# Performance work log

Measured on AMD Instinct MI355X. Metric: run time of the kernel, lower is better.

## Reference

```python
import jax, jax.numpy as jnp
import numpy as np

EPS = 1e-6

def _ln(x):
    m = jnp.mean(x, axis=-1, keepdims=True)
    v = jnp.mean((x - m) ** 2, axis=-1, keepdims=True)
    return (x - m) * jax.lax.rsqrt(v + EPS)

def _quant(x):
    # dynamic per-token symmetric int8 quant (fused_kernels.quant_sum semantics)
    s = jnp.maximum(jnp.max(jnp.abs(x), axis=-1, keepdims=True) / 127.0, 1e-8)
    q = jnp.clip(jnp.round(x / s), -127.0, 127.0)
    return q, s, jnp.sum(q, axis=-1, keepdims=True)

def _w8a8(x, qw, sw, zw, b):
    # W8A8OF16LinearDynamicInputScale: int8 GEMM + zero-point correction via row sum
    q, s, qsum = _quant(x)
    acc = q @ qw.astype(jnp.float32).T - qsum * zw.astype(jnp.float32)
    return acc * (s * sw) + b

def _self_attn(xm, Wqkv, bqkv, Wo, bo, H):
    Bt, S, C = xm.shape
    hd = C // H
    qkv = (xm @ Wqkv.T + bqkv).reshape(Bt, S, 3, H, hd)
    q, k, v = qkv[:, :, 0], qkv[:, :, 1], qkv[:, :, 2]
    attn = jnp.einsum('bqhd,bkhd->bhqk', q * (hd ** -0.5), k).astype(jnp.float32)
    attn = jax.nn.softmax(attn, axis=-1)
    out = jnp.einsum('bhqk,bkhd->bqhd', attn, v).reshape(Bt, S, C)
    return out @ Wo.T + bo

def _cross_attn(x, y, qw_q, sw_q, zw_q, b_q, Wkv, bkv, qw_cp, sw_cp, zw_cp, b_cp, H):
    B, N, C = x.shape
    hd = C // H
    q = _w8a8(x, qw_q, sw_q, zw_q, b_q).reshape(B * N, H, hd)
    kv = (y.reshape(-1, C) @ Wkv.T + bkv).reshape(-1, 2, H, hd)
    k, v = kv[:, 0], kv[:, 1]
    # mask=None path: q (1,B*N,H,hd) attends over all B*M keys (flattened)
    attn = jnp.einsum('qhd,khd->hqk', q * (hd ** -0.5), k).astype(jnp.float32)
    attn = jax.nn.softmax(attn, axis=-1)
    out = jnp.einsum('hqk,khd->qhd', attn, v).reshape(B, N, C)
    return _w8a8(out, qw_cp, sw_cp, zw_cp, b_cp)

def setup_inputs() -> dict:
    key = jax.random.key(0)
    ks = iter(jax.random.split(key, 32))
    B, T, S, C, H, M = 2, 8, 256, 1152, 16, 224
    Dh = int(C * 4.0)
    r = lambda shape, sc=1.0: jax.random.normal(next(ks), shape, dtype=jnp.float32) * sc
    qi = lambda shape: jax.random.randint(next(ks), shape, -127, 128, dtype=jnp.int8)
    zi = lambda shape: jax.random.randint(next(ks), shape, -8, 9, dtype=jnp.int32)
    su = lambda shape: jax.random.uniform(next(ks), shape, minval=0.005, maxval=0.02, dtype=jnp.float32)
    return dict(
        x=r((B, T * S, C)), y=r((B, M, C)), t=r((B, 6 * C)),
        sst=r((6, C), C ** -0.5),
        Wqkv=r((3 * C, C), 0.02), bqkv=r((3 * C,), 0.02),
        Wo=r((C, C), 0.02), bo=r((C,), 0.02),
        Wkv=r((2 * C, C), 0.02), bkv=r((2 * C,), 0.02),
        qw_q=qi((C, C)), sw_q=su((C,)), zw_q=zi((C,)), b_q=r((C,), 0.02),
        qw_cp=qi((C, C)), sw_cp=su((C,)), zw_cp=zi((C,)), b_cp=r((C,), 0.02),
        qw_f1=qi((Dh, C)), sw_f1=su((Dh,)), zw_f1=zi((Dh,)), b_f1=r((Dh,), 0.02),
        qw_f2=qi((C, Dh)), sw_f2=su((C,)), zw_f2=zi((C,)), b_f2=r((C,), 0.02),
        num_heads=H, T=T, S=S,
    )

def reference(x, y, t, sst, Wqkv, bqkv, Wo, bo, Wkv, bkv,
              qw_q, sw_q, zw_q, b_q, qw_cp, sw_cp, zw_cp, b_cp,
              qw_f1, sw_f1, zw_f1, b_f1, qw_f2, sw_f2, zw_f2, b_f2,
              num_heads, T, S):
    B, N, C = x.shape
    mod = sst[None] + t.reshape(B, 6, C)  # (B,6,C)
    shift_msa, scale_msa, gate_msa, shift_mlp, scale_mlp, gate_mlp = (
        mod[:, 0:1], mod[:, 1:2], mod[:, 2:3], mod[:, 3:4], mod[:, 4:5], mod[:, 5:6])
    # --- self-attention (spatial, temporal=False): B (T S) C -> (B T) S C ---
    x_m = _ln(x) * (1.0 + scale_msa) + shift_msa
    x_m = x_m.reshape(B * T, S, C)
    x_m = _self_attn(x_m, Wqkv, bqkv, Wo, bo, num_heads).reshape(B, N, C)
    x = x + gate_msa * x_m  # fused_kernels.gate_residual
    # --- int8 cross-attention ---
    x = x + _cross_attn(x, y, qw_q, sw_q, zw_q, b_q, Wkv, bkv, qw_cp, sw_cp, zw_cp, b_cp, num_heads)
    # --- int8 MLP with fused gelu_quant_sum (tanh-approx GELU) ---
    x_m = _ln(x) * (1.0 + scale_mlp) + shift_mlp
    h = _w8a8(x_m, qw_f1, sw_f1, zw_f1, b_f1)
    h = jax.nn.gelu(h, approximate=True)
    h = _w8a8(h, qw_f2, sw_f2, zw_f2, b_f2)
    x = x + gate_mlp * h
    return x
```

## Files before the change

kernel.cpp:

```cpp
#include <hip/hip_runtime.h>
#include <stdint.h>

typedef unsigned short u16;
typedef _Float16 f16;
typedef f16    f16v8  __attribute__((ext_vector_type(8)));
typedef u16    u16v8  __attribute__((ext_vector_type(8)));
typedef float  f32x4  __attribute__((ext_vector_type(4)));
typedef int    i32x4  __attribute__((ext_vector_type(4)));
typedef int    i32x16 __attribute__((ext_vector_type(16)));

#define MFMA_F16(a,b,c)   __builtin_amdgcn_mfma_f32_16x16x32_f16((a),(b),(c),0,0,0)
#define MFMA_I8_32(a,b,c) __builtin_amdgcn_mfma_i32_32x32x32_i8((a),(b),(c),0,0,0)

__device__ __forceinline__ float b2f(u16 u){ union{unsigned u;float f;}v; v.u=((unsigned)u)<<16; return v.f; }
__device__ __forceinline__ u16 f2b(float f){ union{float f;unsigned u;}v; v.f=f;
  return (u16)((v.u + 0x7fffu + ((v.u>>16)&1u))>>16); }
__device__ __forceinline__ u16 f2h(float f){ f16 h = (f16)f; return __builtin_bit_cast(u16, h); }
__device__ __forceinline__ float h2f(u16 u){ return (float)__builtin_bit_cast(f16, u); }
__device__ __forceinline__ f16v8 ldh8(const u16* p){ return __builtin_bit_cast(f16v8, *(const u16v8*)p); }
__device__ __forceinline__ void gl2lds16(const void* g, void* l){
  __builtin_amdgcn_global_load_lds(
    (const __attribute__((address_space(1))) unsigned int*)g,
    (__attribute__((address_space(3))) unsigned int*)l,
    16, 0, 0);
}
__device__ __forceinline__ float gelu_t(float x){
  float t = tanhf(0.7978845608028654f*(x + 0.044715f*x*x*x));
  return 0.5f*x*(1.0f+t);
}

__global__ void mod_add_k(const float* __restrict__ sst, const float* __restrict__ t, float* __restrict__ mod){
  int i = blockIdx.x*256 + threadIdx.x;
  if (i < 2*6*1152) mod[i] = sst[i % 6912] + t[i];
}
__global__ void split2h_k(const float* __restrict__ src, u16* __restrict__ hi, u16* __restrict__ lo, int n){
  int i = blockIdx.x*256 + threadIdx.x;
  if (i >= n) return;
  float v = src[i];
  f16 h = (f16)v;
  hi[i] = __builtin_bit_cast(u16, h);
  lo[i] = f2h(v - (float)h);
}
__global__ void cross_prep_k(const int* __restrict__ qw_q, int8_t* __restrict__ w8q,
                             const int* __restrict__ qw_cp, int8_t* __restrict__ w8cp,
                             const float* __restrict__ Wkv, u16* __restrict__ wkvh, u16* __restrict__ wkvl,
                             const float* __restrict__ y, u16* __restrict__ yf){
  const int S1 = 1327104, S2 = 2654208, S3 = 5308416, S4 = 5824512;
  int i = blockIdx.x*256 + threadIdx.x;
  if (i < S1){ w8q[i] = (int8_t)qw_q[i]; }
  else if (i < S2){ int j = i - S1; w8cp[j] = (int8_t)qw_cp[j]; }
  else if (i < S3){ int j = i - S2; float v = Wkv[j]; f16 h = (f16)v;
    wkvh[j] = __builtin_bit_cast(u16, h); wkvl[j] = f2h(v - (float)h); }
  else if (i < S4){ int j = i - S3; yf[j] = f2h(y[j]); }
}
__global__ void mlp_prep_k(const int* __restrict__ qw_f1, int8_t* __restrict__ w8f1,
                           const int* __restrict__ qw_f2, int8_t* __restrict__ w8f2){
  const int S1 = 5308416, S2 = 10616832;
  int i = blockIdx.x*256 + threadIdx.x;
  if (i < S1){ w8f1[i] = (int8_t)qw_f1[i]; }
  else if (i < S2){ int j = i - S1; w8f2[j] = (int8_t)qw_f2[j]; }
}
__global__ void ln_mod_f16_k(const float* __restrict__ src, u16* __restrict__ xf,
                             const float* __restrict__ mod, int shift_row, int scale_row){
  const int row = blockIdx.x, tid = threadIdx.x;
  const int b = row >> 11;
  const float* ms = mod + ((size_t)b*6 + shift_row)*1152;
  const float* mc = mod + ((size_t)b*6 + scale_row)*1152;
  __shared__ float r1[256], r2[256];
  float s = 0.f, sq = 0.f, vals[5]; int cnt = 0;
  for (int c = tid; c < 1152; c += 256){
    float v = src[(size_t)row*1152+c];
    vals[cnt++] = v; s += v; sq += v*v;
  }
  r1[tid]=s; r2[tid]=sq; __syncthreads();
  for (int st=128; st>0; st>>=1){ if (tid<st){ r1[tid]+=r1[tid+st]; r2[tid]+=r2[tid+st]; } __syncthreads(); }
  float mean = r1[0]*(1.f/1152.f);
  float var  = r2[0]*(1.f/1152.f) - mean*mean;
  float rstd = rsqrtf(var + 1e-6f);
  cnt = 0;
  for (int c = tid; c < 1152; c += 256){
    float v = (vals[cnt++]-mean)*rstd*(1.f+mc[c]) + ms[c];
    xf[(size_t)row*1152+c] = f2h(v);
  }
}
__global__ void rgq_k(const float* __restrict__ x, const float* __restrict__ ao,
                      const float* __restrict__ mod, int gate_row, float* __restrict__ xw,
                      int8_t* __restrict__ q8, float* __restrict__ s_out, int* __restrict__ q_out){
  const int row = blockIdx.x, tid = threadIdx.x;
  const int b = row >> 11;
  const float* mg = mod + ((size_t)b*6 + gate_row)*1152;
  __shared__ float r1[256];
  __shared__ int ri[256];
  float mx = 0.f, vals[5]; int cnt = 0;
  for (int c = tid; c < 1152; c += 256){
    float v = x[(size_t)row*1152+c] + mg[c]*ao[(size_t)row*1152+c];
    xw[(size_t)row*1152+c] = v;
    vals[cnt++] = v; mx = fmaxf(mx, fabsf(v));
  }
  r1[tid]=mx; __syncthreads();
  for (int st=128; st>0; st>>=1){ if (tid<st) r1[tid]=fmaxf(r1[tid],r1[tid+st]); __syncthreads(); }
  const float s_ = fmaxf(r1[0]*(1.f/127.f), 1e-8f);
  const float inv = 1.f/s_;
  int acc = 0; cnt = 0;
  for (int c = tid; c < 1152; c += 256){
    float q = rintf(vals[cnt++]*inv);
    q = fminf(fmaxf(q, -127.f), 127.f);
    q8[(size_t)row*1152+c] = (int8_t)q;
    acc += (int)q;
  }
  ri[tid]=acc; __syncthreads();
  for (int st=128; st>0; st>>=1){ if (tid<st) ri[tid]+=ri[tid+st]; __syncthreads(); }
  if (tid==0){ s_out[row]=s_; q_out[row]=ri[0]; }
}
__global__ void rlq_k(float* __restrict__ xw, const float* __restrict__ add,
                      const float* __restrict__ mod, int shift_row, int scale_row,
                      int8_t* __restrict__ q8, float* __restrict__ s_out, int* __restrict__ q_out){
  const int row = blockIdx.x, tid = threadIdx.x;
  const int b = row >> 11;
  const float* ms = mod + ((size_t)b*6 + shift_row)*1152;
  const float* mc = mod + ((size_t)b*6 + scale_row)*1152;
  __shared__ float r1[256], r2[256];
  __shared__ int ri[256];
  float s = 0.f, sq = 0.f, vals[5]; int cnt = 0;
  for (int c = tid; c < 1152; c += 256){
    float v = xw[(size_t)row*1152+c] + add[(size_t)row*1152+c];
    xw[(size_t)row*1152+c] = v;
    vals[cnt++] = v; s += v; sq += v*v;
  }
  r1[tid]=s; r2[tid]=sq; __syncthreads();
  for (int st=128; st>0; st>>=1){ if (tid<st){ r1[tid]+=r1[tid+st]; r2[tid]+=r2[tid+st]; } __syncthreads(); }
  float mean = r1[0]*(1.f/1152.f);
  float var  = r2[0]*(1.f/1152.f) - mean*mean;
  float rstd = rsqrtf(var + 1e-6f);
  __syncthreads();
  float mx = 0.f; cnt = 0;
  for (int c = tid; c < 1152; c += 256){
    float v = (vals[cnt]-mean)*rstd*(1.f+mc[c]) + ms[c];
    vals[cnt++] = v; mx = fmaxf(mx, fabsf(v));
  }
  r1[tid]=mx; __syncthreads();
  for (int st=128; st>0; st>>=1){ if (tid<st) r1[tid]=fmaxf(r1[tid],r1[tid+st]); __syncthreads(); }
  const float s_ = fmaxf(r1[0]*(1.f/127.f), 1e-8f);
  const float inv = 1.f/s_;
  int acc = 0; cnt = 0;
  for (int c = tid; c < 1152; c += 256){
    float q = rintf(vals[cnt++]*inv);
    q = fminf(fmaxf(q, -127.f), 127.f);
    q8[(size_t)row*1152+c] = (int8_t)q;
    acc += (int)q;
  }
  ri[tid]=acc; __syncthreads();
  for (int st=128; st>0; st>>=1){ if (tid<st) ri[tid]+=ri[tid+st]; __syncthreads(); }
  if (tid==0){ s_out[row]=s_; q_out[row]=ri[0]; }
}
template<int SRC_F32>
__global__ void quant_rows_k(const void* __restrict__ src, int C_,
                             int8_t* __restrict__ q8, float* __restrict__ s_out, int* __restrict__ q_out){
  const int row = blockIdx.x, tid = threadIdx.x;
  __shared__ float red[256];
  __shared__ int redi[256];
  float vals[18];
  float mx = 0.f; int cnt = 0;
  for (int c = tid; c < C_; c += 256){
    float v = SRC_F32 ? ((const float*)src)[(size_t)row*C_+c] : b2f(((const u16*)src)[(size_t)row*C_+c]);
    vals[cnt++] = v;
    mx = fmaxf(mx, fabsf(v));
  }
  red[tid]=mx; __syncthreads();
  for (int st=128; st>0; st>>=1){ if (tid<st) red[tid]=fmaxf(red[tid],red[tid+st]); __syncthreads(); }
  const float s_ = fmaxf(red[0]*(1.f/127.f), 1e-8f);
  const float inv = 1.f/s_;
  int acc = 0; cnt = 0;
  for (int c = tid; c < C_; c += 256){
    float q = rintf(vals[cnt++]*inv);
    q = fminf(fmaxf(q, -127.f), 127.f);
    q8[(size_t)row*C_+c] = (int8_t)q;
    acc += (int)q;
  }
  redi[tid]=acc; __syncthreads();
  for (int st=128; st>0; st>>=1){ if (tid<st) redi[tid]+=redi[tid+st]; __syncthreads(); }
  if (tid==0){ s_out[row]=s_; q_out[row]=redi[0]; }
}

template<int MODE>
__global__ __launch_bounds__(256,4) void gemm_f16k(
    const u16* __restrict__ Af, int lda,
    const u16* __restrict__ Wh, const u16* __restrict__ Wl, int ldw,
    const float* __restrict__ bias, float* __restrict__ out, int ldo, int M, int K,
    u16* __restrict__ e1, u16* __restrict__ e2){
  __shared__ u16 sA[128*32];
  __shared__ u16 sWh[128*32];
  __shared__ u16 sWl[128*32];
  const int tid = threadIdx.x, lane = tid & 63;
  const int wv = tid >> 6, wx = wv & 1, wy = wv >> 1;
  const int quad = lane >> 4, l16 = lane & 15;
  const int m0 = blockIdx.y*128, n0 = blockIdx.x*128;
  f32x4 acc[4][4];
  #pragma unroll
  for (int i=0;i<4;i++)
    #pragma unroll
    for (int j=0;j<4;j++) acc[i][j] = (f32x4){0.f,0.f,0.f,0.f};
  for (int k0=0; k0<K; k0+=32){
    #pragma unroll
    for (int r=0;r<2;r++){
      int slotbase = r*256 + wv*64;
      int slot = slotbase + lane;
      int row = slot >> 2;
      int col8 = ((slot ^ (row>>1)) & 3) * 8;
      int gm = m0 + row; if (gm > M-1) gm = M-1;
      size_t aoff = (size_t)gm*lda + k0 + col8;
      size_t woff = (size_t)(n0+row)*ldw + k0 + col8;
      gl2lds16(Af + aoff, &sA[(size_t)slotbase*8]);
      gl2lds16(Wh + woff, &sWh[(size_t)slotbase*8]);
      gl2lds16(Wl + woff, &sWl[(size_t)slotbase*8]);
    }
    __syncthreads();
    const int cs = ((quad ^ ((l16>>1)&3)) * 8);
    f16v8 a[4], bh[4], bl[4];
    #pragma unroll
    for (int i=0;i<4;i++) a[i] = ldh8(&sA[(wy*64+i*16+l16)*32 + cs]);
    #pragma unroll
    for (int j=0;j<4;j++){
      bh[j] = ldh8(&sWh[(wx*64+j*16+l16)*32 + cs]);
      bl[j] = ldh8(&sWl[(wx*64+j*16+l16)*32 + cs]);
    }
    #pragma unroll
    for (int i=0;i<4;i++)
      #pragma unroll
      for (int j=0;j<4;j++){
        acc[i][j] = MFMA_F16(a[i], bh[j], acc[i][j]);
        acc[i][j] = MFMA_F16(a[i], bl[j], acc[i][j]);
      }
    __syncthreads();
  }
  #pragma unroll
  for (int j=0;j<4;j++){
    int col = n0 + wx*64 + j*16 + l16;
    float bc = bias ? bias[col] : 0.f;
    #pragma unroll
    for (int i=0;i<4;i++)
      #pragma unroll
      for (int r=0;r<4;r++){
        int row = m0 + wy*64 + i*16 + quad*4 + r;
        if (row >= M) continue;
        float v = acc[i][j][r] + bc;
        if (MODE == 0){
          out[(size_t)row*ldo + col] = v;
        } else if (MODE == 1){
          if (col < 2304){
            e1[(size_t)row*2304 + col] = f2h(v);
          } else {
            int vc = col - 2304;
            int hd_ = vc/72, d = vc - hd_*72;
            int z = row >> 8, s2 = row & 255;
            e2[((size_t)(z*16+hd_)*80 + d)*256 + s2] = f2h(v);
          }
        } else {
          if (col < 1152){
            e1[(size_t)row*1152 + col] = f2h(v);
          } else {
            int vc = col - 1152;
            int hd_ = vc/72, d = vc - hd_*72;
            e2[((size_t)hd_*80 + d)*448 + row] = f2h(v);
          }
        }
      }
  }
}

#define QKV_NT 36
__global__ __launch_bounds__(512,2) void gemm_qkv_8ph(
    const u16* __restrict__ Af,
    const u16* __restrict__ Wh_, const u16* __restrict__ Wl_,
    const float* __restrict__ bias,
    u16* __restrict__ qkf, u16* __restrict__ vtf){
  extern __shared__ u16 sm[];
  char* smb = (char*)sm;
  const int tid = threadIdx.x, lane = tid & 63, wv = tid >> 6;
  const int wr = wv >> 2, wc = wv & 3;
  const int quad = lane >> 4, l16 = lane & 15;
  const int c = blockIdx.x & 7, bi = blockIdx.x >> 3;
  const int m0 = (((c>>1)<<2) + (bi&3)) << 8;
  const int n0 = ((c&1)*7 + (bi>>2)) << 8;

  const u16* gA[2]; const u16* gH[2]; const u16* gL[2];
  int sbase[2];
  #pragma unroll
  for (int r=0;r<2;r++){
    int slot = r*512 + tid;
    int row = slot >> 2;
    int col8 = ((slot ^ (row>>1)) & 3) * 8;
    sbase[r] = (r*512 + wv*64) * 16;
    gA[r] = Af + (size_t)(m0+row)*1152 + col8;
    int gn = n0 + row; if (gn > 3455) gn = 3455;
    gH[r] = Wh_ + (size_t)gn*1152 + col8;
    gL[r] = Wl_ + (size_t)gn*1152 + col8;
  }

  #define STG_A(t2,b) { size_t ko=(size_t)(t2)*32; \
    gl2lds16(gA[0]+ko, smb + (b)*49152 + sbase[0]); \
    gl2lds16(gA[1]+ko, smb + (b)*49152 + sbase[1]); }
  #define STG_H(t2,b) { size_t ko=(size_t)(t2)*32; \
    gl2lds16(gH[0]+ko, smb + (b)*49152 + 16384 + sbase[0]); \
    gl2lds16(gH[1]+ko, smb + (b)*49152 + 16384 + sbase[1]); }
  #define STG_L(t2,b) { size_t ko=(size_t)(t2)*32; \
    gl2lds16(gL[0]+ko, smb + (b)*49152 + 32768 + sbase[0]); \
    gl2lds16(gL[1]+ko, smb + (b)*49152 + 32768 + sbase[1]); }

  STG_A(0,0); STG_H(0,0); STG_L(0,0);
  STG_A(1,1); STG_H(1,1); STG_L(1,1);

  const int cs = (quad ^ ((l16>>1)&3)) * 8;
  const int arow = wr*128 + l16;
  const int wrow = wc*64 + l16;

  f32x4 acc[8][4];
  #pragma unroll
  for (int i=0;i<8;i++)
    #pragma unroll
    for (int j=0;j<4;j++) acc[i][j] = (f32x4){0.f,0.f,0.f,0.f};

  f16v8 bh[4], bl[4];

  #define PHASE(p, STAGE_STMT) { \
    const u16* bA = sm + cur*24576; \
    f16v8 a0 = ldh8(bA + (arow + (2*(p))*16)*32 + cs); \
    f16v8 a1 = ldh8(bA + (arow + (2*(p)+1)*16)*32 + cs); \
    if ((p)==0){ \
      const u16* bH = bA + 8192; \
      const u16* bL = bA + 16384; \
      _Pragma("unroll") \
      for (int j=0;j<4;j++){ \
        bh[j] = ldh8(bH + (wrow + j*16)*32 + cs); \
        bl[j] = ldh8(bL + (wrow + j*16)*32 + cs); \
      } \
    } \
    STAGE_STMT; \
    __builtin_amdgcn_s_barrier(); \
    asm volatile("s_waitcnt lgkmcnt(0)" ::: "memory"); \
    __builtin_amdgcn_sched_barrier(0); \
    __builtin_amdgcn_s_setprio(1); \
    _Pragma("unroll") \
    for (int j=0;j<4;j++){ \
      acc[2*(p)][j]   = MFMA_F16(a0, bh[j], acc[2*(p)][j]); \
      acc[2*(p)][j]   = MFMA_F16(a0, bl[j], acc[2*(p)][j]); \
      acc[2*(p)+1][j] = MFMA_F16(a1, bh[j], acc[2*(p)+1][j]); \
      acc[2*(p)+1][j] = MFMA_F16(a1, bl[j], acc[2*(p)+1][j]); \
    } \
    __builtin_amdgcn_s_setprio(0); \
    __builtin_amdgcn_s_barrier(); \
  }

  int cur = 0;
  for (int t = 0; t < QKV_NT-1; ++t){
    const int nxt = (cur == 0) ? 2 : cur - 1;
    asm volatile("s_waitcnt vmcnt(6)" ::: "memory");
    __builtin_amdgcn_s_barrier();
    __builtin_amdgcn_sched_barrier(0);
    const bool pf = (t < QKV_NT-2);
    PHASE(0, if (pf) STG_A(t+2,nxt));
    PHASE(1, if (pf) STG_H(t+2,nxt));
    PHASE(2, if (pf) STG_L(t+2,nxt));
    PHASE(3, );
    cur = (cur == 2) ? 0 : cur + 1;
  }
  asm volatile("s_waitcnt vmcnt(0)" ::: "memory");
  __builtin_amdgcn_s_barrier();
  __builtin_amdgcn_sched_barrier(0);
  PHASE(0, );
  PHASE(1, );
  PHASE(2, );
  PHASE(3, );

  #pragma unroll
  for (int j=0;j<4;j++){
    const int col = n0 + wc*64 + j*16 + l16;
    if (col < 3456){
      const float bc = bias[col];
      if (col < 2304){
        #pragma unroll
        for (int i=0;i<8;i++){
          const size_t rb = (size_t)(m0 + wr*128 + i*16 + quad*4)*2304 + col;
          #pragma unroll
          for (int r=0;r<4;r++)
            qkf[rb + (size_t)r*2304] = f2h(acc[i][j][r] + bc);
        }
      } else {
        const int vc = col - 2304;
        const int hd_ = vc/72, d = vc - hd_*72;
        #pragma unroll
        for (int i=0;i<8;i++){
          #pragma unroll
          for (int r=0;r<4;r++){
            const int row = m0 + wr*128 + i*16 + quad*4 + r;
            const int z = row >> 8, s2 = row & 255;
            vtf[((size_t)(z*16+hd_)*80 + d)*256 + s2] = f2h(acc[i][j][r] + bc);
          }
        }
      }
    }
  }
  #undef PHASE
  #undef STG_A
  #undef STG_H
  #undef STG_L
}

__global__ __launch_bounds__(256,3) void gemm_i8(
    const int8_t* __restrict__ A, int lda, const int8_t* __restrict__ W, int ldw,
    const float* __restrict__ rs, const int* __restrict__ rq,
    const float* __restrict__ sw, const int* __restrict__ zw, const float* __restrict__ bias,
    void* __restrict__ out, int ldo, int M, int K, int do_gelu, int out_f32,
    const float* __restrict__ xwf, const float* __restrict__ modf, int do_final){
  __shared__ int8_t As[128*128];
  __shared__ int8_t Bs[128*128];
  const int tid = threadIdx.x, lane = tid & 63, wv = tid >> 6;
  const int wx = wv & 1, wy = wv >> 1;
  const int l32 = lane & 31, g = lane >> 5;
  const int m0 = blockIdx.y*128, n0 = blockIdx.x*128;
  const int srow = lane >> 3, schunk = lane & 7;
  const int scol = ((schunk ^ srow) & 7) * 16;
  i32x16 acc[2][2];
  #pragma unroll
  for (int i=0;i<2;i++)
    #pragma unroll
    for (int j=0;j<2;j++)
      #pragma unroll
      for (int r=0;r<16;r++) acc[i][j][r] = 0;
  for (int k0 = 0; k0 < K; k0 += 128){
    #pragma unroll
    for (int i=0;i<4;i++){
      int rr = (i*4 + wv)*8;
      int gm = m0 + rr + srow; if (gm > M-1) gm = M-1;
      gl2lds16(A + (size_t)gm*lda + k0 + scol, &As[rr*128]);
      int gn = n0 + rr + srow;
      gl2lds16(W + (size_t)gn*ldw + k0 + scol, &Bs[rr*128]);
    }
    __syncthreads();
    #pragma unroll
    for (int kq=0; kq<4; kq++){
      i32x4 af[2], bw[2];
      #pragma unroll
      for (int i=0;i<2;i++){
        int row = wy*64 + i*32 + l32;
        int cs = (((kq*2 + g) ^ (row & 7))) * 16;
        af[i] = *(const i32x4*)&As[row*128 + cs];
      }
      #pragma unroll
      for (int j=0;j<2;j++){
        int row = wx*64 + j*32 + l32;
        int cs = (((kq*2 + g) ^ (row & 7))) * 16;
        bw[j] = *(const i32x4*)&Bs[row*128 + cs];
      }
      #pragma unroll
      for (int i=0;i<2;i++)
        #pragma unroll
        for (int j=0;j<2;j++)
          acc[i][j] = MFMA_I8_32(af[i], bw[j], acc[i][j]);
    }
    __syncthreads();
  }
  #pragma unroll
  for (int j=0;j<2;j++){
    int col = n0 + wx*64 + j*32 + l32;
    float swc = sw[col]; float zwc = (float)zw[col]; float bc = bias[col];
    #pragma unroll
    for (int i=0;i<2;i++)
      #pragma unroll
      for (int r=0;r<16;r++){
        int row = m0 + wy*64 + i*32 + (r&3) + 8*(r>>2) + 4*g;
        if (row < M){
          float v = ((float)acc[i][j][r] - (float)rq[row]*zwc) * (rs[row]*swc) + bc;
          if (do_gelu) v = gelu_t(v);
          if (do_final){
            int bb = row >> 11;
            float ov = xwf[(size_t)row*1152 + col] + modf[((size_t)bb*6+5)*1152 + col]*v;
            ((float*)out)[(size_t)row*ldo + col] = ov;
          } else if (out_f32) ((float*)out)[(size_t)row*ldo + col] = v;
          else                ((u16*)out)[(size_t)row*ldo + col] = f2b(v);
        }
      }
  }
}

__global__ __launch_bounds__(256) void attn_self_f16(
    const u16* __restrict__ qkf, const u16* __restrict__ vtf,
    u16* __restrict__ of, float scale){
  constexpr int NT = 16, PSTR = 264, VSTR = 256;
  __shared__ u16 P[4*16*PSTR];
  const int tid = threadIdx.x, lane = tid & 63, wv = tid >> 6;
  const int quad = lane >> 4, l16 = lane & 15;
  const int h = blockIdx.y, z = blockIdx.z;
  const int qbase = z*256 + blockIdx.x*64;
  const u16* Vth = vtf + (size_t)(z*16+h)*80*VSTR;
  const f16v8 zf = __builtin_bit_cast(f16v8, (u16v8)0);
  const int mrow = qbase + wv*16 + l16;

  f16v8 qf[3];
  #pragma unroll
  for (int t=0;t<3;t++){
    if (t==2 && quad!=0){ qf[t]=zf; }
    else qf[t] = ldh8(qkf + (size_t)mrow*2304 + h*72 + t*32 + (t==2?0:quad*8));
  }
  f32x4 sc[NT];
  #pragma unroll
  for (int nt=0; nt<NT; nt++){
    f32x4 a = {0.f,0.f,0.f,0.f};
    #pragma unroll
    for (int t=0;t<3;t++){
      f16v8 kf = zf;
      if (!(t==2 && quad!=0))
        kf = ldh8(qkf + (size_t)(z*256 + nt*16 + l16)*2304 + 1152 + h*72 + t*32 + (t==2?0:quad*8));
      a = MFMA_F16(qf[t], kf, a);
    }
    sc[nt] = a;
  }
  float mx[4] = {-1e30f,-1e30f,-1e30f,-1e30f};
  #pragma unroll
  for (int nt=0; nt<NT; nt++)
    #pragma unroll
    for (int r=0;r<4;r++){ float v = sc[nt][r]*scale; sc[nt][r]=v; mx[r]=fmaxf(mx[r],v); }
  #pragma unroll
  for (int r=0;r<4;r++)
    for (int d=1; d<16; d<<=1) mx[r] = fmaxf(mx[r], __shfl_xor(mx[r], d, 64));
  float sm[4] = {0.f,0.f,0.f,0.f};
  #pragma unroll
  for (int nt=0; nt<NT; nt++)
    #pragma unroll
    for (int r=0;r<4;r++){ float p = __expf(sc[nt][r]-mx[r]); sc[nt][r]=p; sm[r]+=p; }
  #pragma unroll
  for (int r=0;r<4;r++){
    for (int d=1; d<16; d<<=1) sm[r] += __shfl_xor(sm[r], d, 64);
    sm[r] = 1.f/sm[r];
  }
  u16* Pw = P + wv*16*PSTR;
  #pragma unroll
  for (int nt=0; nt<NT; nt++)
    #pragma unroll
    for (int r=0;r<4;r++)
      Pw[(quad*4+r)*PSTR + nt*16 + l16] = f2h(sc[nt][r]*sm[r]);
  const u16* Pr = P + wv*16*PSTR + (size_t)l16*PSTR;
  #pragma unroll
  for (int dt=0; dt<5; dt++){
    f32x4 o = {0.f,0.f,0.f,0.f};
    #pragma unroll
    for (int kk=0; kk<8; kk++){
      f16v8 pv = ldh8(Pr + kk*32 + quad*8);
      f16v8 bv = ldh8(Vth + (size_t)(dt*16+l16)*VSTR + kk*32 + quad*8);
      o = MFMA_F16(pv, bv, o);
    }
    int d = dt*16 + l16;
    if (d < 72){
      #pragma unroll
      for (int r=0;r<4;r++){
        int row = qbase + wv*16 + quad*4 + r;
        of[(size_t)row*1152 + h*72 + d] = f2h(o[r]);
      }
    }
  }
}

__global__ __launch_bounds__(256) void attn_cross_f16(
    const float* __restrict__ Q32,
    const u16* __restrict__ Kf,
    const u16* __restrict__ Vt,
    float* __restrict__ O, float scale){
  constexpr int NT = 28, PSTR = 456, VSTR = 448;
  __shared__ u16 P[4*16*PSTR];
  const int tid = threadIdx.x, lane = tid & 63, wv = tid >> 6;
  const int quad = lane >> 4, l16 = lane & 15;
  const int h = blockIdx.y;
  const int qbase = blockIdx.x*64;
  const u16* Vth = Vt + (size_t)h*80*VSTR;
  const f16v8 zf = __builtin_bit_cast(f16v8, (u16v8)0);

  const int mrow = qbase + wv*16 + l16;
  const float* qp = Q32 + (size_t)mrow*1152 + h*72;
  f16v8 qf[3];
  #pragma unroll
  for (int t=0;t<3;t++){
    if (t==2 && quad!=0){ qf[t]=zf; continue; }
    u16v8 hv;
    #pragma unroll
    for (int j=0;j<8;j++) hv[j] = f2h(qp[t*32 + (t==2?0:quad*8) + j]);
    qf[t] = __builtin_bit_cast(f16v8, hv);
  }
  f32x4 sc[NT];
  #pragma unroll
  for (int nt=0; nt<NT; nt++){
    f32x4 a = {0.f,0.f,0.f,0.f};
    #pragma unroll
    for (int t=0;t<3;t++){
      f16v8 kf = zf;
      if (!(t==2 && quad!=0))
        kf = ldh8(Kf + (size_t)(nt*16 + l16)*1152 + h*72 + t*32 + (t==2?0:quad*8));
      a = MFMA_F16(qf[t], kf, a);
    }
    sc[nt] = a;
  }
  float mx[4] = {-1e30f,-1e30f,-1e30f,-1e30f};
  #pragma unroll
  for (int nt=0; nt<NT; nt++)
    #pragma unroll
    for (int r=0;r<4;r++){ float v = sc[nt][r]*scale; sc[nt][r]=v; mx[r]=fmaxf(mx[r],v); }
  #pragma unroll
  for (int r=0;r<4;r++)
    for (int d=1; d<16; d<<=1) mx[r] = fmaxf(mx[r], __shfl_xor(mx[r], d, 64));
  float sm[4] = {0.f,0.f,0.f,0.f};
  #pragma unroll
  for (int nt=0; nt<NT; nt++)
    #pragma unroll
    for (int r=0;r<4;r++){ float p = __expf(sc[nt][r]-mx[r]); sc[nt][r]=p; sm[r]+=p; }
  #pragma unroll
  for (int r=0;r<4;r++){
    for (int d=1; d<16; d<<=1) sm[r] += __shfl_xor(sm[r], d, 64);
    sm[r] = 1.f/sm[r];
  }
  u16* Pw = P + wv*16*PSTR;
  #pragma unroll
  for (int nt=0; nt<NT; nt++)
    #pragma unroll
    for (int r=0;r<4;r++)
      Pw[(quad*4+r)*PSTR + nt*16 + l16] = f2h(sc[nt][r]*sm[r]);
  const u16* Pr = P + wv*16*PSTR + (size_t)l16*PSTR;
  #pragma unroll
  for (int dt=0; dt<5; dt++){
    f32x4 o = {0.f,0.f,0.f,0.f};
    #pragma unroll
    for (int kk=0; kk<14; kk++){
      f16v8 pv = ldh8(Pr + kk*32 + quad*8);
      f16v8 bv = ldh8(Vth + (size_t)(dt*16+l16)*VSTR + kk*32 + quad*8);
      o = MFMA_F16(pv, bv, o);
    }
    int d = dt*16 + l16;
    if (d < 72){
      #pragma unroll
      for (int r=0;r<4;r++){
        int row = qbase + wv*16 + quad*4 + r;
        O[(size_t)row*1152 + h*72 + d] = o[r];
      }
    }
  }
}

extern "C" void kernel_launch(void* const* d_in, const int* in_sizes, int n_in,
                              void* d_out, int out_size, void* d_ws, size_t ws_size,
                              hipStream_t stream){
  const float* x    = (const float*)d_in[0];
  const float* y    = (const float*)d_in[1];
  const float* t    = (const float*)d_in[2];
  const float* sst  = (const float*)d_in[3];
  const float* Wqkv = (const float*)d_in[4];
  const float* bqkv = (const float*)d_in[5];
  const float* Wo   = (const float*)d_in[6];
  const float* bo   = (const float*)d_in[7];
  const float* Wkv  = (const float*)d_in[8];
  const float* bkv  = (const float*)d_in[9];
  const int*   qw_q  = (const int*)d_in[10];
  const float* sw_q  = (const float*)d_in[11];
  const int*   zw_q  = (const int*)d_in[12];
  const float* b_q   = (const float*)d_in[13];
  const int*   qw_cp = (const int*)d_in[14];
  const float* sw_cp = (const float*)d_in[15];
  const int*   zw_cp = (const int*)d_in[16];
  const float* b_cp  = (const float*)d_in[17];
  const int*   qw_f1 = (const int*)d_in[18];
  const float* sw_f1 = (const float*)d_in[19];
  const int*   zw_f1 = (const int*)d_in[20];
  const float* b_f1  = (const float*)d_in[21];
  const int*   qw_f2 = (const int*)d_in[22];
  const float* sw_f2 = (const float*)d_in[23];
  const int*   zw_f2 = (const int*)d_in[24];
  const float* b_f2  = (const float*)d_in[25];
  (void)in_sizes; (void)n_in; (void)out_size;

  constexpr size_t SZR = (size_t)4096*1152*4;
  constexpr size_t R0 = 0;
  constexpr size_t R1 = R0 + SZR;
  constexpr size_t R2 = R1 + SZR;
  constexpr size_t R3 = R2 + SZR;
  constexpr size_t R4 = R3 + SZR;
  constexpr size_t R5 = R4 + (size_t)9437184;
  constexpr size_t R6 = R5 + (size_t)9437184;
  constexpr size_t RS = R6 + (size_t)10485760;
  constexpr size_t RQ = RS + (size_t)4096*4;
  constexpr size_t RM = RQ + (size_t)4096*4;
  constexpr size_t WS_NEED = RM + (size_t)2*6*1152*4;
  if (ws_size < WS_NEED) return;

  char* ws = (char*)d_ws;
  float*  xw    = (float*)(ws + R0);
  u16*    wqkvh = (u16*)(ws + R1);
  u16*    wqkvl = (u16*)(ws + R1 + (size_t)3456*1152*2);
  u16*    wkvh  = (u16*)(ws + R1);
  u16*    wkvl  = (u16*)(ws + R1 + (size_t)2304*1152*2);
  u16*    yf    = (u16*)(ws + R1 + (size_t)2*2304*1152*2);
  float*  q32   = (float*)(ws + R1);
  float*  cpout = (float*)(ws + R1);
  int8_t* q8h   = (int8_t*)(ws + R1);
  u16*    qkf   = (u16*)(ws + R2);
  float*  aof   = (float*)(ws + R2);
  u16*    hbuf  = (u16*)(ws + R2);
  u16*    xmf   = (u16*)(ws + R4);
  u16*    of    = (u16*)(ws + R4);
  u16*    kf    = (u16*)(ws + R4 + (size_t)4128768);
  u16*    vtc   = (u16*)(ws + R4 + (size_t)6193152);
  int8_t* w8f2  = (int8_t*)(ws + R4);
  int8_t* w8q   = (int8_t*)(ws + R5);
  int8_t* w8cp  = (int8_t*)(ws + R5 + (size_t)1327104);
  int8_t* w8f1  = (int8_t*)(ws + R5 + (size_t)2654208);
  u16*    vtf   = (u16*)(ws + R6);
  u16*    woh   = (u16*)(ws + R6);
  u16*    wol   = (u16*)(ws + R6 + (size_t)1152*1152*2);
  int8_t* q8x   = (int8_t*)(ws + R6);
  float*  rs    = (float*)(ws + RS);
  int*    rq    = (int*)(ws + RQ);
  float*  mod   = (float*)(ws + RM);

  const float scale = 0.11785113019775793f;

  static bool attr_set = false;
  if (!attr_set){
    hipFuncSetAttribute(reinterpret_cast<const void*>(gemm_qkv_8ph),
                        hipFuncAttributeMaxDynamicSharedMemorySize, 3*49152);
    attr_set = true;
  }

  mod_add_k<<<(2*6*1152+255)/256,256,0,stream>>>(sst, t, mod);

  ln_mod_f16_k<<<4096,256,0,stream>>>(x, xmf, mod, 0, 1);
  split2h_k<<<(3456*1152+255)/256,256,0,stream>>>(Wqkv, wqkvh, wqkvl, 3456*1152);
  gemm_qkv_8ph<<<dim3(224),dim3(512),3*49152,stream>>>(xmf, wqkvh, wqkvl, bqkv, qkf, vtf);
  attn_self_f16<<<dim3(4,16,16),256,0,stream>>>(qkf, vtf, of, scale);
  split2h_k<<<(1152*1152+255)/256,256,0,stream>>>(Wo, woh, wol, 1152*1152);
  gemm_f16k<0><<<dim3(9,32),256,0,stream>>>(of,1152, woh,wol,1152, bo, aof,1152, 4096,1152, nullptr,nullptr);
  rgq_k<<<4096,256,0,stream>>>(x, aof, mod, 2, xw, q8x, rs, rq);

  cross_prep_k<<<(5824512+255)/256,256,0,stream>>>(qw_q,w8q, qw_cp,w8cp, Wkv,wkvh,wkvl, y,yf);
  gemm_f16k<2><<<dim3(18,4),256,0,stream>>>(yf,1152, wkvh,wkvl,1152, bkv, nullptr,0, 448,1152, kf,vtc);
  gemm_i8<<<dim3(9,32),256,0,stream>>>(q8x,1152, w8q,1152, rs,rq, sw_q,zw_q,b_q, q32,1152, 4096,1152, 0, 1, nullptr,nullptr,0);
  attn_cross_f16<<<dim3(64,16),256,0,stream>>>(q32, kf, vtc, aof, scale);
  quant_rows_k<1><<<4096,256,0,stream>>>(aof, 1152, q8x, rs, rq);
  gemm_i8<<<dim3(9,32),256,0,stream>>>(q8x,1152, w8cp,1152, rs,rq, sw_cp,zw_cp,b_cp, cpout,1152, 4096,1152, 0, 1, nullptr,nullptr,0);

  rlq_k<<<4096,256,0,stream>>>(xw, cpout, mod, 3, 4, q8x, rs, rq);
  mlp_prep_k<<<(10616832+255)/256,256,0,stream>>>(qw_f1, w8f1, qw_f2, w8f2);
  gemm_i8<<<dim3(36,32),256,0,stream>>>(q8x,1152, w8f1,1152, rs,rq, sw_f1,zw_f1,b_f1, hbuf,4608, 4096,1152, 1, 0, nullptr,nullptr,0);
  quant_rows_k<0><<<4096,256,0,stream>>>(hbuf, 4608, q8h, rs, rq);
  gemm_i8<<<dim3(9,32),256,0,stream>>>(q8h,4608, w8f2,4608, rs,rq, sw_f2,zw_f2,b_f2, d_out,1152, 4096,4608, 0, 1, xw,mod,1);
}
```

Before: 791.5 us.

## Double-buffer int8 GEMM LDS tiles with async prefetch of next K-slab

The int8 GEMM now keeps two LDS buffers for A and W and issues the global-to-LDS loads for the next 128-wide K slab before computing on the current one. Partial vmcnt waits and raw s_barrier replace the two full __syncthreads per iteration. LDS fragment loads are batched in pairs with s_setprio raised around the MFMA bursts. Doubling the LDS tiles to 64KB drops the occupancy hint from 3 to 2 blocks per CU, trading latency hiding across waves for overlap within a block.

```diff
diff --git a/kernel.cpp b/kernel.cpp
--- a/kernel.cpp
+++ b/kernel.cpp
@@ -406,20 +406,37 @@
   #undef STG_L
 }
 
-__global__ __launch_bounds__(256,3) void gemm_i8(
+__global__ __launch_bounds__(256,2) void gemm_i8(
     const int8_t* __restrict__ A, int lda, const int8_t* __restrict__ W, int ldw,
     const float* __restrict__ rs, const int* __restrict__ rq,
     const float* __restrict__ sw, const int* __restrict__ zw, const float* __restrict__ bias,
     void* __restrict__ out, int ldo, int M, int K, int do_gelu, int out_f32,
     const float* __restrict__ xwf, const float* __restrict__ modf, int do_final){
-  __shared__ int8_t As[128*128];
-  __shared__ int8_t Bs[128*128];
+  __shared__ int8_t As[2][128*128];
+  __shared__ int8_t Bs[2][128*128];
   const int tid = threadIdx.x, lane = tid & 63, wv = tid >> 6;
   const int wx = wv & 1, wy = wv >> 1;
   const int l32 = lane & 31, g = lane >> 5;
   const int m0 = blockIdx.y*128, n0 = blockIdx.x*128;
   const int srow = lane >> 3, schunk = lane & 7;
   const int scol = ((schunk ^ srow) & 7) * 16;
+
+  const int8_t* gA[4]; const int8_t* gB[4]; int lb[4];
+  #pragma unroll
+  for (int i=0;i<4;i++){
+    int rr = (i*4 + wv)*8;
+    int gm = m0 + rr + srow; if (gm > M-1) gm = M-1;
+    int gn = n0 + rr + srow;
+    gA[i] = A + (size_t)gm*lda + scol;
+    gB[i] = W + (size_t)gn*ldw + scol;
+    lb[i] = rr*128;
+  }
+  #define STAGE_I8(kk,b) { int ko=(kk); \
+    _Pragma("unroll") \
+    for (int i=0;i<4;i++){ \
+      gl2lds16(gA[i]+ko, &As[b][lb[i]]); \
+      gl2lds16(gB[i]+ko, &Bs[b][lb[i]]); } }
+
   i32x16 acc[2][2];
   #pragma unroll
   for (int i=0;i<2;i++)
@@ -427,39 +444,54 @@
     for (int j=0;j<2;j++)
       #pragma unroll
       for (int r=0;r<16;r++) acc[i][j][r] = 0;
-  for (int k0 = 0; k0 < K; k0 += 128){
-    #pragma unroll
-    for (int i=0;i<4;i++){
-      int rr = (i*4 + wv)*8;
-      int gm = m0 + rr + srow; if (gm > M-1) gm = M-1;
-      gl2lds16(A + (size_t)gm*lda + k0 + scol, &As[rr*128]);
-      int gn = n0 + rr + srow;
-      gl2lds16(W + (size_t)gn*ldw + k0 + scol, &Bs[rr*128]);
-    }
-    __syncthreads();
-    #pragma unroll
-    for (int kq=0; kq<4; kq++){
-      i32x4 af[2], bw[2];
+
+  const int NK = K >> 7;
+  STAGE_I8(0, 0);
+  int cur = 0;
+  for (int t = 0; t < NK; ++t){
+    if (t+1 < NK){
+      STAGE_I8((t+1)*128, cur^1);
+      asm volatile("s_waitcnt vmcnt(8)" ::: "memory");
+    } else {
+      asm volatile("s_waitcnt vmcnt(0)" ::: "memory");
+    }
+    __builtin_amdgcn_s_barrier();
+    __builtin_amdgcn_sched_barrier(0);
+    #pragma unroll
+    for (int ph=0; ph<2; ph++){
+      i32x4 af[2][2], bw[2][2];
       #pragma unroll
-      for (int i=0;i<2;i++){
-        int row = wy*64 + i*32 + l32;
-        int cs = (((kq*2 + g) ^ (row & 7))) * 16;
-        af[i] = *(const i32x4*)&As[row*128 + cs];
+      for (int hh=0; hh<2; hh++){
+        const int kq = ph*2 + hh;
+        #pragma unroll
+        for (int i=0;i<2;i++){
+          int row = wy*64 + i*32 + l32;
+          int cs2 = (((kq*2 + g) ^ (row & 7))) * 16;
+          af[hh][i] = *(const i32x4*)&As[cur][row*128 + cs2];
+        }
+        #pragma unroll
+        for (int j=0;j<2;j++){
+          int row = wx*64 + j*32 + l32;
+          int cs2 = (((kq*2 + g) ^ (row & 7))) * 16;
+          bw[hh][j] = *(const i32x4*)&Bs[cur][row*128 + cs2];
+        }
       }
+      asm volatile("s_waitcnt lgkmcnt(0)" ::: "memory");
+      __builtin_amdgcn_sched_barrier(0);
+      __builtin_amdgcn_s_setprio(1);
       #pragma unroll
-      for (int j=0;j<2;j++){
-        int row = wx*64 + j*32 + l32;
-        int cs = (((kq*2 + g) ^ (row & 7))) * 16;
-        bw[j] = *(const i32x4*)&Bs[row*128 + cs];
-      }
-      #pragma unroll
-      for (int i=0;i<2;i++)
+      for (int hh=0; hh<2; hh++)
         #pragma unroll
-        for (int j=0;j<2;j++)
-          acc[i][j] = MFMA_I8_32(af[i], bw[j], acc[i][j]);
-    }
-    __syncthreads();
-  }
+        for (int i=0;i<2;i++)
+          #pragma unroll
+          for (int j=0;j<2;j++)
+            acc[i][j] = MFMA_I8_32(af[hh][i], bw[hh][j], acc[i][j]);
+      __builtin_amdgcn_s_setprio(0);
+    }
+    __builtin_amdgcn_s_barrier();
+    cur ^= 1;
+  }
+
   #pragma unroll
   for (int j=0;j<2;j++){
     int col = n0 + wx*64 + j*32 + l32;
@@ -481,6 +513,7 @@
         }
       }
   }
+  #undef STAGE_I8
 }
 
 __global__ __launch_bounds__(256) void attn_self_f16(
```

After: 808.0 us. 1.02x slower.
